# Kernel tuning notes

Hardware: AMD Instinct MI355X
Metric: run time of the kernel (lower is better)

Reference implementation:

```python
import jax, jax.numpy as jnp
import numpy as np

B, SEQ, D, H = 4, 128, 64, 512
EPS = 1e-6


def setup_inputs() -> dict:
    key = jax.random.key(0)
    ks = jax.random.split(key, 7)
    sc = lambda fan_in: 1.0 / np.sqrt(fan_in)
    return {
        "x": jax.random.normal(ks[0], (B, SEQ, D), dtype=jnp.float32),
        "W1": jax.random.normal(ks[1], (D, H), dtype=jnp.float32) * sc(D),
        "b1": jax.random.normal(ks[2], (H,), dtype=jnp.float32) * sc(D),
        "W2": jax.random.normal(ks[3], (H, H), dtype=jnp.float32) * sc(H),
        "b2": jax.random.normal(ks[4], (H,), dtype=jnp.float32) * sc(H),
        "W3": jax.random.normal(ks[5], (H, D * D), dtype=jnp.float32) * sc(H),
        "b3": jax.random.normal(ks[6], (D * D,), dtype=jnp.float32) * sc(H),
    }


def _geometry(x, W1, b1, W2, b2, W3, b3):
    d = W1.shape[0]
    # LearnableMetricTensor: MLP on mean-pooled tokens -> Cholesky-like PD metric
    h = x.mean(axis=1)                                  # [B, d]
    h = jax.nn.relu(h @ W1 + b1)
    h = jax.nn.relu(h @ W2 + b2)
    L = jnp.tril((h @ W3 + b3).reshape(-1, d, d))       # [B, d, d]
    G = L @ jnp.swapaxes(L, -1, -2) + EPS * jnp.eye(d, dtype=x.dtype)
    Ginv = jnp.linalg.inv(G)

    # Christoffel symbols (vectorized form of the per-(i,j,k) loop):
    # Gamma[b,i,j,k] = 0.5 * sum_m Ginv[b,i,m] * (G[b,(m-1)%d,k] + G[b,j,(m-1)%d] - G[b,j,k])
    A = jnp.roll(G, 1, axis=1)                          # A[b,m,k] = G[b,(m-1)%d,k]
    Bm = jnp.roll(G, 1, axis=2)                         # Bm[b,j,m] = G[b,j,(m-1)%d]
    T1 = jnp.einsum('bim,bmk->bik', Ginv, A)            # depends on (i,k)
    T2 = jnp.einsum('bim,bjm->bij', Ginv, Bm)           # depends on (i,j)
    s = Ginv.sum(axis=-1)                               # [B, i]
    Gamma = 0.5 * (T1[:, :, None, :] + T2[:, :, :, None]
                   - s[:, :, None, None] * G[:, None, :, :])  # [B, i, j, k]

    # Riemann tensor (vectorized form of the quadruple loop):
    # partial terms use torch.roll along the batch dim, as in the source
    Dp = jnp.roll(Gamma, 1, axis=0) - Gamma             # Dp[b,i,j,l]
    conn1 = jnp.einsum('bimk,bmjl->bijkl', Gamma, Gamma)
    riemann = (Dp[:, :, :, None, :] - Dp[:, :, :, :, None]
               + conn1 - jnp.swapaxes(conn1, 3, 4))      # [B, i, j, k, l]

    ricci = jnp.einsum('bkikj->bij', riemann)
    scalar_curv = jnp.einsum('bij,bij->b', ricci, Ginv)
    return G, Gamma, riemann, ricci, scalar_curv


def reference(x, W1, b1, W2, b2, W3, b3):
    G, Gamma, riemann, ricci, scalar_curv = _geometry(x, W1, b1, W2, b2, W3, b3)
    return (G, Gamma, riemann, ricci, scalar_curv, x)
```

## Files before the change

kernel.cpp:

```cpp
#include <hip/hip_runtime.h>


#define EPSF 1e-6f

typedef unsigned short u16;
typedef __attribute__((ext_vector_type(8))) short short8v;
typedef __attribute__((ext_vector_type(4))) float f32x4v;
typedef __attribute__((ext_vector_type(2))) double d64x2;

__device__ __forceinline__ u16 f2bf_rne(float f) {
  unsigned u = __float_as_uint(f);
  return (u16)((u + 0x7FFFu + ((u >> 16) & 1u)) >> 16);
}

__global__ void k_mlp_a(const float* __restrict__ x,
                        const float* __restrict__ W1, const float* __restrict__ b1,
                        float* __restrict__ h1out) {
  int b = blockIdx.x;
  int t = threadIdx.x;
  __shared__ float h0[64];
  if (t < 64) {
    const float* xb = x + b * 8192;
    float s = 0.f;
    #pragma unroll 8
    for (int q = 0; q < 128; ++q) s += xb[q * 64 + t];
    h0[t] = s * (1.f / 128.f);
  }
  __syncthreads();
  float acc = b1[t];
  #pragma unroll 8
  for (int d = 0; d < 64; ++d) acc = fmaf(h0[d], W1[d * 512 + t], acc);
  h1out[b * 512 + t] = fmaxf(acc, 0.f);
}

__global__ void k_h2(const float* __restrict__ h1all, const float* __restrict__ W2,
                     const float* __restrict__ b2, float* __restrict__ h2out) {
  int o0 = blockIdx.x * 64, b = blockIdx.y;
  int t = threadIdx.x;
  __shared__ float h1[512];
  __shared__ float red[4][64];
  for (int k = t; k < 512; k += 256) h1[k] = h1all[b * 512 + k];
  __syncthreads();
  int o = o0 + (t & 63), q = t >> 6;
  float acc = 0.f;
  #pragma unroll 8
  for (int k = q * 128; k < q * 128 + 128; ++k)
    acc = fmaf(h1[k], W2[k * 512 + o], acc);
  red[q][t & 63] = acc;
  __syncthreads();
  if (t < 64) {
    float v = red[0][t] + red[1][t] + red[2][t] + red[3][t] + b2[o0 + t];
    h2out[b * 512 + o0 + t] = fmaxf(v, 0.f);
  }
}

__global__ void k_L2(const float* __restrict__ h2all, const float* __restrict__ W3,
                     const float* __restrict__ b3, float* __restrict__ Lout) {
  int t = threadIdx.x;
  int le = t & 127, half = t >> 7;
  int e = blockIdx.x * 128 + le;
  __shared__ float h[4][512];
  __shared__ float red[4][2][128];
  for (int k = t; k < 2048; k += 256) h[k >> 9][k & 511] = h2all[k];
  __syncthreads();
  int i = e >> 6, j = e & 63;
  float a0 = 0.f, a1 = 0.f, a2 = 0.f, a3 = 0.f;
  if (j <= i) {
    const float* w = W3 + (size_t)half * 256 * 4096 + e;
    const float* hh = &h[0][half * 256];
    #pragma unroll 8
    for (int k = 0; k < 256; ++k) {
      float wv = w[(size_t)k * 4096];
      a0 = fmaf(hh[k], wv, a0);
      a1 = fmaf(hh[512 + k], wv, a1);
      a2 = fmaf(hh[1024 + k], wv, a2);
      a3 = fmaf(hh[1536 + k], wv, a3);
    }
  }
  red[0][half][le] = a0; red[1][half][le] = a1;
  red[2][half][le] = a2; red[3][half][le] = a3;
  __syncthreads();
  if (half == 0) {
    float keep = (j <= i) ? 1.f : 0.f;
    float bb = keep * b3[e];
    #pragma unroll
    for (int bi = 0; bi < 4; ++bi)
      Lout[bi * 4096 + e] = keep * (red[bi][0][le] + red[bi][1][le]) + bb;
  }
}

__global__ void k_G(const float* __restrict__ Lin, float* __restrict__ Gout) {
  int b = blockIdx.x;
  __shared__ float Ls[64 * 65];
  for (int e = threadIdx.x; e < 4096; e += 256)
    Ls[(e >> 6) * 65 + (e & 63)] = Lin[b * 4096 + e];
  __syncthreads();
  for (int p = 0; p < 16; ++p) {
    int e = p * 256 + threadIdx.x;
    int i = e >> 6, j = e & 63;
    float acc = (i == j) ? EPSF : 0.f;
    for (int k = 0; k < 64; ++k) acc = fmaf(Ls[i * 65 + k], Ls[j * 65 + k], acc);
    Gout[b * 4096 + e] = acc;
  }
}

__global__ void k_inv(const float* __restrict__ G, float* __restrict__ Ginv) {
  int b = blockIdx.x;
  int t = threadIdx.x;
  __shared__ double M[64][128];
  __shared__ double prbuf[2][128];
  __shared__ double pvbuf[2];
  int cl = (t & 63) * 2;
  int R0 = (t >> 6) * 16;
  for (int e = t; e < 64 * 128; e += 256) {
    int i = e >> 7, jj = e & 127;
    double v;
    if (jj < 64) v = (double)G[b * 4096 + i * 64 + jj];
    else         v = (jj - 64 == i) ? 1.0 : 0.0;
    M[i][jj] = v;
  }
  __syncthreads();
  if (t < 64) {
    prbuf[0][2 * t]     = M[0][2 * t];
    prbuf[0][2 * t + 1] = M[0][2 * t + 1];
  }
  if (t == 0) pvbuf[0] = M[0][0];
  __syncthreads();
  for (int p = 0; p < 64; ++p) {
    int cur = p & 1, nxt = cur ^ 1;
    double pv   = pvbuf[cur];
    double prv0 = prbuf[cur][cl];
    double prv1 = prbuf[cur][cl + 1];
    double fac[16];
    d64x2 av[16];
    #pragma unroll
    for (int q = 0; q < 16; ++q) fac[q] = M[R0 + q][p];
    #pragma unroll
    for (int q = 0; q < 16; ++q) av[q] = *(const d64x2*)&M[R0 + q][cl];
    double pivinv = 1.0 / pv;
    #pragma unroll
    for (int q = 0; q < 16; ++q) {
      int r = R0 + q;
      double f = (r == p) ? (1.0 - pivinv) : fac[q] * pivinv;
      double n0 = av[q].x - f * prv0;
      double n1 = av[q].y - f * prv1;
      d64x2 nv; nv.x = n0; nv.y = n1;
      *(d64x2*)&M[r][cl] = nv;
      if (r == p + 1) {
        prbuf[nxt][cl]     = n0;
        prbuf[nxt][cl + 1] = n1;
        if (cl == ((p + 1) & 62)) pvbuf[nxt] = ((p + 1) & 1) ? n1 : n0;
      }
    }
    __syncthreads();
  }
  for (int e = t; e < 4096; e += 256)
    Ginv[b * 4096 + e] = (float)M[e >> 6][64 + (e & 63)];
}

__global__ void k_gamma2(const float* __restrict__ G, const float* __restrict__ Ginv,
                         float* __restrict__ GammaOut) {
  int i = blockIdx.x, b = blockIdx.y;
  int t = threadIdx.x;
  __shared__ float Gs[64 * 65];
  __shared__ float gi[64];
  __shared__ float T1[64];
  __shared__ float T2[64];
  __shared__ float svs;
  for (int e = t; e < 4096; e += 256)
    Gs[(e >> 6) * 65 + (e & 63)] = G[b * 4096 + e];
  if (t < 64) gi[t] = Ginv[b * 4096 + i * 64 + t];
  __syncthreads();
  if (t < 64) {
    float acc = 0.f, acc2 = 0.f;
    #pragma unroll 8
    for (int m = 0; m < 64; ++m) {
      acc  = fmaf(gi[m], Gs[((m - 1) & 63) * 65 + t], acc);
      acc2 = fmaf(gi[m], Gs[t * 65 + ((m - 1) & 63)], acc2);
    }
    T1[t] = acc;
    T2[t] = acc2;
    if (t == 0) {
      float s = 0.f;
      for (int m = 0; m < 64; ++m) s += gi[m];
      svs = s;
    }
  }
  __syncthreads();
  float sv = svs;
  float* o = GammaOut + b * 262144 + i * 4096;
  #pragma unroll
  for (int p = 0; p < 16; ++p) {
    int e = p * 256 + t;
    int jj = e >> 6, k = e & 63;
    o[e] = 0.5f * (T1[k] + T2[jj] - sv * Gs[jj * 65 + k]);
  }
}

__global__ void k_prep2(const float* __restrict__ Gamma,
                        u16* __restrict__ Tah, u16* __restrict__ Tal,
                        u16* __restrict__ Tbh, u16* __restrict__ Tbl,
                        const float* __restrict__ x, float* __restrict__ Xout) {
  int s = blockIdx.x, b = blockIdx.y;
  int t = threadIdx.x;
  __shared__ float Ls[64 * 65];
  {
    int gblk = b * 64 + s;
    if (t < 128) Xout[gblk * 128 + t] = x[gblk * 128 + t];
  }
  const float* Gb = Gamma + b * 262144;
  int base = (b * 64 + s) << 12;
  for (int p = 0; p < 16; ++p) {
    int e = p * 256 + t;
    Ls[(e >> 6) * 65 + (e & 63)] = Gb[s * 4096 + e];
  }
  __syncthreads();
  for (int p = 0; p < 16; ++p) {
    int e = p * 256 + t;
    int k = e >> 6, m = e & 63;
    float f = Ls[m * 65 + k];
    u16 hi = f2bf_rne(f);
    float fl = f - __uint_as_float(((unsigned)hi) << 16);
    u16 lo = f2bf_rne(fl);
    Tah[base + e] = hi;
    Tal[base + e] = lo;
  }
  __syncthreads();
  for (int p = 0; p < 16; ++p) {
    int e = p * 256 + t;
    int m = e >> 6, l = e & 63;
    Ls[m * 65 + l] = Gb[m * 4096 + s * 64 + l];
  }
  __syncthreads();
  for (int p = 0; p < 16; ++p) {
    int e = p * 256 + t;
    int l = e >> 6, m = e & 63;
    float f = Ls[m * 65 + l];
    u16 hi = f2bf_rne(f);
    float fl = f - __uint_as_float(((unsigned)hi) << 16);
    u16 lo = f2bf_rne(fl);
    int idx = base + l * 64 + (((m >> 3) ^ (l & 7)) << 3) + (m & 7);
    Tbh[idx] = hi;
    Tbl[idx] = lo;
  }
}

__global__ void k_riemann2(const float* __restrict__ Gamma,
                           const u16* __restrict__ Tah, const u16* __restrict__ Tal,
                           const u16* __restrict__ Tbh, const u16* __restrict__ Tbl,
                           float* __restrict__ R) {
  int j = blockIdx.x, i = blockIdx.y, b = blockIdx.z;
  int t = threadIdx.x;
  __shared__ __align__(16) char smem[64 * 68 * 4];
  __shared__ float dvec[64];
  u16* sBh = (u16*)smem;
  u16* sBl = sBh + 4096;
  float* sU = (float*)smem;

  {
    const u16* pbh = Tbh + ((b * 64 + j) << 12);
    const u16* pbl = Tbl + ((b * 64 + j) << 12);
    #pragma unroll
    for (int p = 0; p < 2; ++p) {
      int g = (p << 8) + t;
      *(short8v*)(sBh + (g << 3)) = *(const short8v*)(pbh + (g << 3));
      *(short8v*)(sBl + (g << 3)) = *(const short8v*)(pbl + (g << 3));
    }
  }
  if (t < 64) {
    const float* Gp = Gamma + ((b + 3) & 3) * 262144 + i * 4096 + j * 64;
    const float* Gc = Gamma + b * 262144 + i * 4096 + j * 64;
    dvec[t] = Gp[t] - Gc[t];
  }

  int lane = t & 63, wv = t >> 6;
  int li = lane & 15, lg = lane >> 4;
  const u16* tah = Tah + (((b * 64 + i) << 12) + (16 * wv + li) * 64 + 8 * lg);
  const u16* tal = Tal + (((b * 64 + i) << 12) + (16 * wv + li) * 64 + 8 * lg);
  short8v aH0 = *(const short8v*)(tah);
  short8v aH1 = *(const short8v*)(tah + 32);
  short8v aL0 = *(const short8v*)(tal);
  short8v aL1 = *(const short8v*)(tal + 32);

  __syncthreads();

  f32x4v acc[4];
  #pragma unroll
  for (int tc = 0; tc < 4; ++tc) {
    acc[tc] = (f32x4v){0.f, 0.f, 0.f, 0.f};
    int rb = 16 * tc + li;
    int rx = rb & 7;
    int off0 = rb * 64 + ((lg ^ rx) << 3);
    int off1 = rb * 64 + (((4 + lg) ^ rx) << 3);
    short8v bH0 = *(const short8v*)(sBh + off0);
    short8v bL0 = *(const short8v*)(sBl + off0);
    short8v bH1 = *(const short8v*)(sBh + off1);
    short8v bL1 = *(const short8v*)(sBl + off1);
    acc[tc] = __builtin_amdgcn_mfma_f32_16x16x32_bf16(aH0, bH0, acc[tc], 0, 0, 0);
    acc[tc] = __builtin_amdgcn_mfma_f32_16x16x32_bf16(aL0, bH0, acc[tc], 0, 0, 0);
    acc[tc] = __builtin_amdgcn_mfma_f32_16x16x32_bf16(aH0, bL0, acc[tc], 0, 0, 0);
    acc[tc] = __builtin_amdgcn_mfma_f32_16x16x32_bf16(aH1, bH1, acc[tc], 0, 0, 0);
    acc[tc] = __builtin_amdgcn_mfma_f32_16x16x32_bf16(aL1, bH1, acc[tc], 0, 0, 0);
    acc[tc] = __builtin_amdgcn_mfma_f32_16x16x32_bf16(aH1, bL1, acc[tc], 0, 0, 0);
  }
  __syncthreads();
  #pragma unroll
  for (int tc = 0; tc < 4; ++tc) {
    #pragma unroll
    for (int r = 0; r < 4; ++r)
      sU[(16 * wv + 4 * lg + r) * 68 + 16 * tc + li] = acc[tc][r];
  }
  __syncthreads();

  int tx = t & 15, ty = t >> 4;
  int l0 = 4 * tx, k0 = 4 * ty;
  float mir[4][4];
  #pragma unroll
  for (int r = 0; r < 4; ++r) {
    float4 v = *(const float4*)(sU + (l0 + r) * 68 + k0);
    mir[r][0] = v.x; mir[r][1] = v.y; mir[r][2] = v.z; mir[r][3] = v.w;
  }
  float dl0 = dvec[l0], dl1 = dvec[l0 + 1], dl2 = dvec[l0 + 2], dl3 = dvec[l0 + 3];
  float* Rout = R + (((size_t)((b * 64 + i) * 64 + j)) << 12);
  #pragma unroll
  for (int q = 0; q < 4; ++q) {
    float4 uq = *(const float4*)(sU + (k0 + q) * 68 + l0);
    float dk = dvec[k0 + q];
    float4 o;
    o.x = uq.x - mir[0][q] + dl0 - dk;
    o.y = uq.y - mir[1][q] + dl1 - dk;
    o.z = uq.z - mir[2][q] + dl2 - dk;
    o.w = uq.w - mir[3][q] + dl3 - dk;
    *(float4*)(Rout + (k0 + q) * 64 + l0) = o;
  }
}

__global__ void k_riemann_f32(const float* __restrict__ Gamma, float* __restrict__ R) {
  int j = blockIdx.x, i = blockIdx.y, b = blockIdx.z;
  int t = threadIdx.x;
  __shared__ float Ai[64 * 64];
  __shared__ float Bj[64 * 64];
  __shared__ float U[64 * 65];
  __shared__ float dvec[64];
  const float* Gb = Gamma + b * 262144;
  const float* Gbi = Gb + i * 4096;
  for (int e = t; e < 4096; e += 256) Ai[e] = Gbi[e];
  for (int e = t; e < 4096; e += 256) {
    int m = e >> 6, l = e & 63;
    Bj[e] = Gb[m * 4096 + j * 64 + l];
  }
  if (t < 64) {
    const float* Gp = Gamma + ((b + 3) & 3) * 262144 + i * 4096 + j * 64;
    dvec[t] = Gp[t] - Gbi[j * 64 + t];
  }
  __syncthreads();
  int tx = t & 15, ty = t >> 4;
  int k0 = ty * 4, l0 = tx * 4;
  float acc[4][4] = {{0.f}};
  for (int m = 0; m < 64; ++m) {
    float4 a = *(const float4*)(Ai + m * 64 + k0);
    float4 bb = *(const float4*)(Bj + m * 64 + l0);
    acc[0][0] = fmaf(a.x, bb.x, acc[0][0]); acc[0][1] = fmaf(a.x, bb.y, acc[0][1]);
    acc[0][2] = fmaf(a.x, bb.z, acc[0][2]); acc[0][3] = fmaf(a.x, bb.w, acc[0][3]);
    acc[1][0] = fmaf(a.y, bb.x, acc[1][0]); acc[1][1] = fmaf(a.y, bb.y, acc[1][1]);
    acc[1][2] = fmaf(a.y, bb.z, acc[1][2]); acc[1][3] = fmaf(a.y, bb.w, acc[1][3]);
    acc[2][0] = fmaf(a.z, bb.x, acc[2][0]); acc[2][1] = fmaf(a.z, bb.y, acc[2][1]);
    acc[2][2] = fmaf(a.z, bb.z, acc[2][2]); acc[2][3] = fmaf(a.z, bb.w, acc[2][3]);
    acc[3][0] = fmaf(a.w, bb.x, acc[3][0]); acc[3][1] = fmaf(a.w, bb.y, acc[3][1]);
    acc[3][2] = fmaf(a.w, bb.z, acc[3][2]); acc[3][3] = fmaf(a.w, bb.w, acc[3][3]);
  }
  for (int q = 0; q < 4; ++q)
    for (int r = 0; r < 4; ++r)
      U[(k0 + q) * 65 + (l0 + r)] = acc[q][r];
  __syncthreads();
  float* Rout = R + (((size_t)((b * 64 + i) * 64 + j)) << 12);
  for (int q = 0; q < 4; ++q) {
    int k = k0 + q;
    float dk = dvec[k];
    float4 o;
    o.x = acc[q][0] - U[(l0 + 0) * 65 + k] + dvec[l0 + 0] - dk;
    o.y = acc[q][1] - U[(l0 + 1) * 65 + k] + dvec[l0 + 1] - dk;
    o.z = acc[q][2] - U[(l0 + 2) * 65 + k] + dvec[l0 + 2] - dk;
    o.w = acc[q][3] - U[(l0 + 3) * 65 + k] + dvec[l0 + 3] - dk;
    *(float4*)(Rout + k * 64 + l0) = o;
  }
}

__global__ void k_ricci3(const float* __restrict__ Gamma, float* __restrict__ ricci) {
  int i = blockIdx.x, b = blockIdx.y;
  int t = threadIdx.x;
  int j = t & 63, q = t >> 6;
  __shared__ float sC[64][65];
  __shared__ float redA[4][64];
  __shared__ float redS[4][64];
  __shared__ float redP[4][64];
  __shared__ float sPc[64];
  __shared__ float tmpP[64];
  const float* Gb = Gamma + b * 262144;
  int bp = (b + 3) & 3;
  const float* Gp = Gamma + bp * 262144;
  for (int e = t; e < 4096; e += 256) {
    int m = e >> 6, k = e & 63;
    sC[m][k] = Gb[m * 4096 + i * 64 + k];
  }
  if (t < 64) tmpP[t] = Gp[t * 4096 + i * 64 + t];
  __syncthreads();
  float a4p = 0.f, sgp = 0.f, pcp = 0.f;
  for (int mm = 0; mm < 16; ++mm) {
    int m = q * 16 + mm;
    const float* col = Gb + m * 64 + j;
    float partial = 0.f;
    #pragma unroll 8
    for (int k = 0; k < 64; ++k)
      partial = fmaf(sC[m][k], col[(size_t)k * 4096], partial);
    a4p += partial;
    sgp += Gp[m * 4096 + i * 64 + j];
    pcp += Gb[m * 4097 + j * 64];
  }
  redA[q][j] = a4p;
  redS[q][j] = sgp;
  redP[q][j] = pcp;
  __syncthreads();
  if (t < 64) sPc[t] = redP[0][t] + redP[1][t] + redP[2][t] + redP[3][t];
  __syncthreads();
  if (t < 64) {
    float a4  = redA[0][t] + redA[1][t] + redA[2][t] + redA[3][t];
    float SGp = redS[0][t] + redS[1][t] + redS[2][t] + redS[3][t];
    float SGc = 0.f, a3 = 0.f;
    #pragma unroll 8
    for (int m = 0; m < 64; ++m) {
      SGc += sC[m][t];
      a3 = fmaf(sPc[m], sC[m][t], a3);
    }
    float Ppi = 0.f;
    #pragma unroll 8
    for (int s = 0; s < 64; ++s) Ppi += tmpP[s];
    ricci[b * 4096 + i * 64 + t] = (SGp - SGc) - (Ppi - sPc[i]) + a3 - a4;
  }
}

__global__ void k_scal(const float* __restrict__ ricci, const float* __restrict__ Ginv,
                       float* __restrict__ scal) {
  int b = blockIdx.x;
  int t = threadIdx.x;
  __shared__ float red[256];
  float local = 0.f;
  for (int e = t; e < 4096; e += 256) local += ricci[b * 4096 + e] * Ginv[b * 4096 + e];
  red[t] = local;
  __syncthreads();
  for (int off = 128; off > 0; off >>= 1) {
    if (t < off) red[t] += red[t + off];
    __syncthreads();
  }
  if (t == 0) scal[b] = red[0];
}

__global__ void k_copy(const float* __restrict__ x, float* __restrict__ out) {
  int idx = blockIdx.x * 256 + threadIdx.x;
  out[idx] = x[idx];
}

extern "C" void kernel_launch(void* const* d_in, const int* in_sizes, int n_in,
                              void* d_out, int out_size, void* d_ws, size_t ws_size,
                              hipStream_t stream) {
  const float* x  = (const float*)d_in[0];
  const float* W1 = (const float*)d_in[1];
  const float* b1 = (const float*)d_in[2];
  const float* W2 = (const float*)d_in[3];
  const float* b2 = (const float*)d_in[4];
  const float* W3 = (const float*)d_in[5];
  const float* b3 = (const float*)d_in[6];

  float* out   = (float*)d_out;
  float* G     = out;
  float* Gamma = out + 16384;
  float* Riem  = out + 1064960;
  float* Ricci = out + 68173824;
  float* Scal  = out + 68190208;
  float* Xout  = out + 68190212;

  float* ws   = (float*)d_ws;
  float* h1   = ws;
  float* Lbuf = ws + 2048;
  float* h2   = ws + 18432;
  float* Ginv = ws + 18432;
  u16* Tah = (u16*)(ws + 34816);
  u16* Tal = Tah + (1 << 20);
  u16* Tbh = Tal + (1 << 20);
  u16* Tbl = Tbh + (1 << 20);
  const size_t need = 34816u * 4u + 4u * (1u << 21);

  hipLaunchKernelGGL(k_mlp_a, dim3(4),     dim3(512), 0, stream, x, W1, b1, h1);
  hipLaunchKernelGGL(k_h2,    dim3(8, 4),  dim3(256), 0, stream, h1, W2, b2, h2);
  hipLaunchKernelGGL(k_L2,    dim3(32),    dim3(256), 0, stream, h2, W3, b3, Lbuf);
  hipLaunchKernelGGL(k_G,     dim3(4),     dim3(256), 0, stream, Lbuf, G);
  hipLaunchKernelGGL(k_inv,   dim3(4),     dim3(256), 0, stream, G, Ginv);
  hipLaunchKernelGGL(k_gamma2, dim3(64, 4), dim3(256), 0, stream, G, Ginv, Gamma);
  hipLaunchKernelGGL(k_ricci3, dim3(64, 4), dim3(256), 0, stream, Gamma, Ricci);
  hipLaunchKernelGGL(k_scal,   dim3(4),     dim3(256), 0, stream, Ricci, Ginv, Scal);
  if (ws_size >= need) {
    hipLaunchKernelGGL(k_prep2,    dim3(64, 4),     dim3(256), 0, stream,
                       Gamma, Tah, Tal, Tbh, Tbl, x, Xout);
    hipLaunchKernelGGL(k_riemann2, dim3(64, 64, 4), dim3(256), 0, stream,
                       Gamma, Tah, Tal, Tbh, Tbl, Riem);
  } else {
    hipLaunchKernelGGL(k_copy,        dim3(128),       dim3(256), 0, stream, x, Xout);
    hipLaunchKernelGGL(k_riemann_f32, dim3(64, 64, 4), dim3(256), 0, stream, Gamma, Riem);
  }
}
```

Baseline: 267.1 us.

## Fuse small kernels to cut launches and fold bf16 split prep into producers

Merges the two front MLP layers into one kernel (recomputing layer 1 per block), folds the x copy into the W3 kernel, merges G construction with the fp64 Gauss-Jordan inverse using a shared-memory union, and moves the bf16 hi/lo split of Gamma into the gamma and ricci kernels so the separate prep pass and its re-read of Gamma disappear. The aim is to reduce kernel launch count and redundant global traffic in a latency-dominated chain. In exchange, the layer-1 work is recomputed in every block, and the gamma and ricci kernels do extra stores.

```diff
diff --git a/kernel.cpp b/kernel.cpp
--- a/kernel.cpp
+++ b/kernel.cpp
@@ -13,12 +13,15 @@
   return (u16)((u + 0x7FFFu + ((u >> 16) & 1u)) >> 16);
 }
 
-__global__ void k_mlp_a(const float* __restrict__ x,
-                        const float* __restrict__ W1, const float* __restrict__ b1,
-                        float* __restrict__ h1out) {
-  int b = blockIdx.x;
+__global__ void k_front2(const float* __restrict__ x,
+                         const float* __restrict__ W1, const float* __restrict__ b1,
+                         const float* __restrict__ W2, const float* __restrict__ b2,
+                         float* __restrict__ h2out) {
+  int o0 = blockIdx.x * 64, b = blockIdx.y;
   int t = threadIdx.x;
   __shared__ float h0[64];
+  __shared__ float h1[512];
+  __shared__ float red[4][64];
   if (t < 64) {
     const float* xb = x + b * 8192;
     float s = 0.f;
@@ -27,19 +30,12 @@
     h0[t] = s * (1.f / 128.f);
   }
   __syncthreads();
-  float acc = b1[t];
-  #pragma unroll 8
-  for (int d = 0; d < 64; ++d) acc = fmaf(h0[d], W1[d * 512 + t], acc);
-  h1out[b * 512 + t] = fmaxf(acc, 0.f);
-}
-
-__global__ void k_h2(const float* __restrict__ h1all, const float* __restrict__ W2,
-                     const float* __restrict__ b2, float* __restrict__ h2out) {
-  int o0 = blockIdx.x * 64, b = blockIdx.y;
-  int t = threadIdx.x;
-  __shared__ float h1[512];
-  __shared__ float red[4][64];
-  for (int k = t; k < 512; k += 256) h1[k] = h1all[b * 512 + k];
+  for (int k = t; k < 512; k += 256) {
+    float acc = b1[k];
+    #pragma unroll 8
+    for (int d = 0; d < 64; ++d) acc = fmaf(h0[d], W1[d * 512 + k], acc);
+    h1[k] = fmaxf(acc, 0.f);
+  }
   __syncthreads();
   int o = o0 + (t & 63), q = t >> 6;
   float acc = 0.f;
@@ -54,9 +50,14 @@
   }
 }
 
-__global__ void k_L2(const float* __restrict__ h2all, const float* __restrict__ W3,
-                     const float* __restrict__ b3, float* __restrict__ Lout) {
-  int t = threadIdx.x;
+__global__ void k_L2x(const float* __restrict__ h2all, const float* __restrict__ W3,
+                      const float* __restrict__ b3, float* __restrict__ Lout,
+                      const float* __restrict__ x, float* __restrict__ Xout) {
+  int t = threadIdx.x;
+  {
+    int idx = blockIdx.x * 1024 + t * 4;
+    *(float4*)(Xout + idx) = *(const float4*)(x + idx);
+  }
   int le = t & 127, half = t >> 7;
   int e = blockIdx.x * 128 + le;
   __shared__ float h[4][512];
@@ -89,54 +90,56 @@
   }
 }
 
-__global__ void k_G(const float* __restrict__ Lin, float* __restrict__ Gout) {
+__global__ void k_invG(const float* __restrict__ Lin, float* __restrict__ Gout,
+                       float* __restrict__ Ginv) {
   int b = blockIdx.x;
-  __shared__ float Ls[64 * 65];
-  for (int e = threadIdx.x; e < 4096; e += 256)
-    Ls[(e >> 6) * 65 + (e & 63)] = Lin[b * 4096 + e];
-  __syncthreads();
+  int t = threadIdx.x;
+  __shared__ union {
+    float Ls[64 * 65];
+    struct { double M[64][128]; double prbuf[2][128]; double pvbuf[2]; } inv;
+  } sm;
+  for (int e = t; e < 4096; e += 256)
+    sm.Ls[(e >> 6) * 65 + (e & 63)] = Lin[b * 4096 + e];
+  __syncthreads();
+  float Gv[16];
+  #pragma unroll
   for (int p = 0; p < 16; ++p) {
-    int e = p * 256 + threadIdx.x;
+    int e = p * 256 + t;
     int i = e >> 6, j = e & 63;
     float acc = (i == j) ? EPSF : 0.f;
-    for (int k = 0; k < 64; ++k) acc = fmaf(Ls[i * 65 + k], Ls[j * 65 + k], acc);
+    #pragma unroll 8
+    for (int k = 0; k < 64; ++k) acc = fmaf(sm.Ls[i * 65 + k], sm.Ls[j * 65 + k], acc);
+    Gv[p] = acc;
     Gout[b * 4096 + e] = acc;
   }
-}
-
-__global__ void k_inv(const float* __restrict__ G, float* __restrict__ Ginv) {
-  int b = blockIdx.x;
-  int t = threadIdx.x;
-  __shared__ double M[64][128];
-  __shared__ double prbuf[2][128];
-  __shared__ double pvbuf[2];
+  __syncthreads();
+  #pragma unroll
+  for (int p = 0; p < 16; ++p) {
+    int e = p * 256 + t;
+    int i = e >> 6, j = e & 63;
+    sm.inv.M[i][j] = (double)Gv[p];
+    sm.inv.M[i][64 + j] = (i == j) ? 1.0 : 0.0;
+  }
+  __syncthreads();
+  if (t < 64) {
+    sm.inv.prbuf[0][2 * t]     = sm.inv.M[0][2 * t];
+    sm.inv.prbuf[0][2 * t + 1] = sm.inv.M[0][2 * t + 1];
+  }
+  if (t == 0) sm.inv.pvbuf[0] = sm.inv.M[0][0];
+  __syncthreads();
   int cl = (t & 63) * 2;
   int R0 = (t >> 6) * 16;
-  for (int e = t; e < 64 * 128; e += 256) {
-    int i = e >> 7, jj = e & 127;
-    double v;
-    if (jj < 64) v = (double)G[b * 4096 + i * 64 + jj];
-    else         v = (jj - 64 == i) ? 1.0 : 0.0;
-    M[i][jj] = v;
-  }
-  __syncthreads();
-  if (t < 64) {
-    prbuf[0][2 * t]     = M[0][2 * t];
-    prbuf[0][2 * t + 1] = M[0][2 * t + 1];
-  }
-  if (t == 0) pvbuf[0] = M[0][0];
-  __syncthreads();
   for (int p = 0; p < 64; ++p) {
     int cur = p & 1, nxt = cur ^ 1;
-    double pv   = pvbuf[cur];
-    double prv0 = prbuf[cur][cl];
-    double prv1 = prbuf[cur][cl + 1];
+    double pv   = sm.inv.pvbuf[cur];
+    double prv0 = sm.inv.prbuf[cur][cl];
+    double prv1 = sm.inv.prbuf[cur][cl + 1];
     double fac[16];
     d64x2 av[16];
     #pragma unroll
-    for (int q = 0; q < 16; ++q) fac[q] = M[R0 + q][p];
-    #pragma unroll
-    for (int q = 0; q < 16; ++q) av[q] = *(const d64x2*)&M[R0 + q][cl];
+    for (int q = 0; q < 16; ++q) fac[q] = sm.inv.M[R0 + q][p];
+    #pragma unroll
+    for (int q = 0; q < 16; ++q) av[q] = *(const d64x2*)&sm.inv.M[R0 + q][cl];
     double pivinv = 1.0 / pv;
     #pragma unroll
     for (int q = 0; q < 16; ++q) {
@@ -145,24 +148,26 @@
       double n0 = av[q].x - f * prv0;
       double n1 = av[q].y - f * prv1;
       d64x2 nv; nv.x = n0; nv.y = n1;
-      *(d64x2*)&M[r][cl] = nv;
+      *(d64x2*)&sm.inv.M[r][cl] = nv;
       if (r == p + 1) {
-        prbuf[nxt][cl]     = n0;
-        prbuf[nxt][cl + 1] = n1;
-        if (cl == ((p + 1) & 62)) pvbuf[nxt] = ((p + 1) & 1) ? n1 : n0;
+        sm.inv.prbuf[nxt][cl]     = n0;
+        sm.inv.prbuf[nxt][cl + 1] = n1;
+        if (cl == ((p + 1) & 62)) sm.inv.pvbuf[nxt] = ((p + 1) & 1) ? n1 : n0;
       }
     }
     __syncthreads();
   }
   for (int e = t; e < 4096; e += 256)
-    Ginv[b * 4096 + e] = (float)M[e >> 6][64 + (e & 63)];
-}
-
-__global__ void k_gamma2(const float* __restrict__ G, const float* __restrict__ Ginv,
-                         float* __restrict__ GammaOut) {
+    Ginv[b * 4096 + e] = (float)sm.inv.M[e >> 6][64 + (e & 63)];
+}
+
+__global__ void k_gamma3(const float* __restrict__ G, const float* __restrict__ Ginv,
+                         float* __restrict__ GammaOut,
+                         u16* __restrict__ Tah, u16* __restrict__ Tal) {
   int i = blockIdx.x, b = blockIdx.y;
   int t = threadIdx.x;
   __shared__ float Gs[64 * 65];
+  __shared__ float Tt[64 * 65];
   __shared__ float gi[64];
   __shared__ float T1[64];
   __shared__ float T2[64];
@@ -193,56 +198,110 @@
   for (int p = 0; p < 16; ++p) {
     int e = p * 256 + t;
     int jj = e >> 6, k = e & 63;
-    o[e] = 0.5f * (T1[k] + T2[jj] - sv * Gs[jj * 65 + k]);
-  }
-}
-
-__global__ void k_prep2(const float* __restrict__ Gamma,
-                        u16* __restrict__ Tah, u16* __restrict__ Tal,
-                        u16* __restrict__ Tbh, u16* __restrict__ Tbl,
-                        const float* __restrict__ x, float* __restrict__ Xout) {
-  int s = blockIdx.x, b = blockIdx.y;
-  int t = threadIdx.x;
-  __shared__ float Ls[64 * 65];
-  {
-    int gblk = b * 64 + s;
-    if (t < 128) Xout[gblk * 128 + t] = x[gblk * 128 + t];
-  }
+    float val = 0.5f * (T1[k] + T2[jj] - sv * Gs[jj * 65 + k]);
+    o[e] = val;
+    Tt[jj * 65 + k] = val;
+  }
+  __syncthreads();
+  if (Tah) {
+    int base = (b * 64 + i) << 12;
+    #pragma unroll
+    for (int p = 0; p < 16; ++p) {
+      int e = p * 256 + t;
+      int k = e >> 6, m = e & 63;
+      float f = Tt[m * 65 + k];
+      u16 hi = f2bf_rne(f);
+      float fl = f - __uint_as_float(((unsigned)hi) << 16);
+      u16 lo = f2bf_rne(fl);
+      Tah[base + e] = hi;
+      Tal[base + e] = lo;
+    }
+  }
+}
+
+__global__ void k_ricci4(const float* __restrict__ Gamma, float* __restrict__ ricci,
+                         u16* __restrict__ Tbh, u16* __restrict__ Tbl) {
+  int i = blockIdx.x, b = blockIdx.y;
+  int t = threadIdx.x;
+  int j = t & 63, q = t >> 6;
+  __shared__ float sC[64][65];
+  __shared__ float redA[4][64];
+  __shared__ float redS[4][64];
+  __shared__ float redP[4][64];
+  __shared__ float sPc[64];
+  __shared__ float tmpP[64];
   const float* Gb = Gamma + b * 262144;
-  int base = (b * 64 + s) << 12;
-  for (int p = 0; p < 16; ++p) {
-    int e = p * 256 + t;
-    Ls[(e >> 6) * 65 + (e & 63)] = Gb[s * 4096 + e];
-  }
-  __syncthreads();
-  for (int p = 0; p < 16; ++p) {
-    int e = p * 256 + t;
-    int k = e >> 6, m = e & 63;
-    float f = Ls[m * 65 + k];
-    u16 hi = f2bf_rne(f);
-    float fl = f - __uint_as_float(((unsigned)hi) << 16);
-    u16 lo = f2bf_rne(fl);
-    Tah[base + e] = hi;
-    Tal[base + e] = lo;
-  }
-  __syncthreads();
-  for (int p = 0; p < 16; ++p) {
-    int e = p * 256 + t;
-    int m = e >> 6, l = e & 63;
-    Ls[m * 65 + l] = Gb[m * 4096 + s * 64 + l];
-  }
-  __syncthreads();
-  for (int p = 0; p < 16; ++p) {
-    int e = p * 256 + t;
-    int l = e >> 6, m = e & 63;
-    float f = Ls[m * 65 + l];
-    u16 hi = f2bf_rne(f);
-    float fl = f - __uint_as_float(((unsigned)hi) << 16);
-    u16 lo = f2bf_rne(fl);
-    int idx = base + l * 64 + (((m >> 3) ^ (l & 7)) << 3) + (m & 7);
-    Tbh[idx] = hi;
-    Tbl[idx] = lo;
-  }
+  int bp = (b + 3) & 3;
+  const float* Gp = Gamma + bp * 262144;
+  for (int e = t; e < 4096; e += 256) {
+    int m = e >> 6, k = e & 63;
+    sC[m][k] = Gb[m * 4096 + i * 64 + k];
+  }
+  if (t < 64) tmpP[t] = Gp[t * 4096 + i * 64 + t];
+  __syncthreads();
+  float a4p = 0.f, sgp = 0.f, pcp = 0.f;
+  for (int mm = 0; mm < 16; ++mm) {
+    int m = q * 16 + mm;
+    const float* col = Gb + m * 64 + j;
+    float partial = 0.f;
+    #pragma unroll 8
+    for (int k = 0; k < 64; ++k)
+      partial = fmaf(sC[m][k], col[(size_t)k * 4096], partial);
+    a4p += partial;
+    sgp += Gp[m * 4096 + i * 64 + j];
+    pcp += Gb[m * 4097 + j * 64];
+  }
+  redA[q][j] = a4p;
+  redS[q][j] = sgp;
+  redP[q][j] = pcp;
+  __syncthreads();
+  if (t < 64) sPc[t] = redP[0][t] + redP[1][t] + redP[2][t] + redP[3][t];
+  __syncthreads();
+  if (t < 64) {
+    float a4  = redA[0][t] + redA[1][t] + redA[2][t] + redA[3][t];
+    float SGp = redS[0][t] + redS[1][t] + redS[2][t] + redS[3][t];
+    float SGc = 0.f, a3 = 0.f;
+    #pragma unroll 8
+    for (int m = 0; m < 64; ++m) {
+      SGc += sC[m][t];
+      a3 = fmaf(sPc[m], sC[m][t], a3);
+    }
+    float Ppi = 0.f;
+    #pragma unroll 8
+    for (int s = 0; s < 64; ++s) Ppi += tmpP[s];
+    ricci[b * 4096 + i * 64 + t] = (SGp - SGc) - (Ppi - sPc[i]) + a3 - a4;
+  }
+  if (Tbh) {
+    int base = (b * 64 + i) << 12;
+    #pragma unroll
+    for (int p = 0; p < 16; ++p) {
+      int e = p * 256 + t;
+      int l = e >> 6, m = e & 63;
+      float f = sC[m][l];
+      u16 hi = f2bf_rne(f);
+      float fl = f - __uint_as_float(((unsigned)hi) << 16);
+      u16 lo = f2bf_rne(fl);
+      int idx = base + l * 64 + (((m >> 3) ^ (l & 7)) << 3) + (m & 7);
+      Tbh[idx] = hi;
+      Tbl[idx] = lo;
+    }
+  }
+}
+
+__global__ void k_scal(const float* __restrict__ ricci, const float* __restrict__ Ginv,
+                       float* __restrict__ scal) {
+  int b = blockIdx.x;
+  int t = threadIdx.x;
+  __shared__ float red[256];
+  float local = 0.f;
+  for (int e = t; e < 4096; e += 256) local += ricci[b * 4096 + e] * Ginv[b * 4096 + e];
+  red[t] = local;
+  __syncthreads();
+  for (int off = 128; off > 0; off >>= 1) {
+    if (t < off) red[t] += red[t + off];
+    __syncthreads();
+  }
+  if (t == 0) scal[b] = red[0];
 }
 
 __global__ void k_riemann2(const float* __restrict__ Gamma,
@@ -386,80 +445,6 @@
   }
 }
 
-__global__ void k_ricci3(const float* __restrict__ Gamma, float* __restrict__ ricci) {
-  int i = blockIdx.x, b = blockIdx.y;
-  int t = threadIdx.x;
-  int j = t & 63, q = t >> 6;
-  __shared__ float sC[64][65];
-  __shared__ float redA[4][64];
-  __shared__ float redS[4][64];
-  __shared__ float redP[4][64];
-  __shared__ float sPc[64];
-  __shared__ float tmpP[64];
-  const float* Gb = Gamma + b * 262144;
-  int bp = (b + 3) & 3;
-  const float* Gp = Gamma + bp * 262144;
-  for (int e = t; e < 4096; e += 256) {
-    int m = e >> 6, k = e & 63;
-    sC[m][k] = Gb[m * 4096 + i * 64 + k];
-  }
-  if (t < 64) tmpP[t] = Gp[t * 4096 + i * 64 + t];
-  __syncthreads();
-  float a4p = 0.f, sgp = 0.f, pcp = 0.f;
-  for (int mm = 0; mm < 16; ++mm) {
-    int m = q * 16 + mm;
-    const float* col = Gb + m * 64 + j;
-    float partial = 0.f;
-    #pragma unroll 8
-    for (int k = 0; k < 64; ++k)
-      partial = fmaf(sC[m][k], col[(size_t)k * 4096], partial);
-    a4p += partial;
-    sgp += Gp[m * 4096 + i * 64 + j];
-    pcp += Gb[m * 4097 + j * 64];
-  }
-  redA[q][j] = a4p;
-  redS[q][j] = sgp;
-  redP[q][j] = pcp;
-  __syncthreads();
-  if (t < 64) sPc[t] = redP[0][t] + redP[1][t] + redP[2][t] + redP[3][t];
-  __syncthreads();
-  if (t < 64) {
-    float a4  = redA[0][t] + redA[1][t] + redA[2][t] + redA[3][t];
-    float SGp = redS[0][t] + redS[1][t] + redS[2][t] + redS[3][t];
-    float SGc = 0.f, a3 = 0.f;
-    #pragma unroll 8
-    for (int m = 0; m < 64; ++m) {
-      SGc += sC[m][t];
-      a3 = fmaf(sPc[m], sC[m][t], a3);
-    }
-    float Ppi = 0.f;
-    #pragma unroll 8
-    for (int s = 0; s < 64; ++s) Ppi += tmpP[s];
-    ricci[b * 4096 + i * 64 + t] = (SGp - SGc) - (Ppi - sPc[i]) + a3 - a4;
-  }
-}
-
-__global__ void k_scal(const float* __restrict__ ricci, const float* __restrict__ Ginv,
-                       float* __restrict__ scal) {
-  int b = blockIdx.x;
-  int t = threadIdx.x;
-  __shared__ float red[256];
-  float local = 0.f;
-  for (int e = t; e < 4096; e += 256) local += ricci[b * 4096 + e] * Ginv[b * 4096 + e];
-  red[t] = local;
-  __syncthreads();
-  for (int off = 128; off > 0; off >>= 1) {
-    if (t < off) red[t] += red[t + off];
-    __syncthreads();
-  }
-  if (t == 0) scal[b] = red[0];
-}
-
-__global__ void k_copy(const float* __restrict__ x, float* __restrict__ out) {
-  int idx = blockIdx.x * 256 + threadIdx.x;
-  out[idx] = x[idx];
-}
-
 extern "C" void kernel_launch(void* const* d_in, const int* in_sizes, int n_in,
                               void* d_out, int out_size, void* d_ws, size_t ws_size,
                               hipStream_t stream) {
@@ -480,31 +465,28 @@
   float* Xout  = out + 68190212;
 
   float* ws   = (float*)d_ws;
-  float* h1   = ws;
+  float* h2   = ws;
   float* Lbuf = ws + 2048;
-  float* h2   = ws + 18432;
   float* Ginv = ws + 18432;
   u16* Tah = (u16*)(ws + 34816);
   u16* Tal = Tah + (1 << 20);
   u16* Tbh = Tal + (1 << 20);
   u16* Tbl = Tbh + (1 << 20);
   const size_t need = 34816u * 4u + 4u * (1u << 21);
-
-  hipLaunchKernelGGL(k_mlp_a, dim3(4),     dim3(512), 0, stream, x, W1, b1, h1);
-  hipLaunchKernelGGL(k_h2,    dim3(8, 4),  dim3(256), 0, stream, h1, W2, b2, h2);
-  hipLaunchKernelGGL(k_L2,    dim3(32),    dim3(256), 0, stream, h2, W3, b3, Lbuf);
-  hipLaunchKernelGGL(k_G,     dim3(4),     dim3(256), 0, stream, Lbuf, G);
-  hipLaunchKernelGGL(k_inv,   dim3(4),     dim3(256), 0, stream, G, Ginv);
-  hipLaunchKernelGGL(k_gamma2, dim3(64, 4), dim3(256), 0, stream, G, Ginv, Gamma);
-  hipLaunchKernelGGL(k_ricci3, dim3(64, 4), dim3(256), 0, stream, Gamma, Ricci);
+  bool mfma = (ws_size >= need);
+
+  hipLaunchKernelGGL(k_front2, dim3(8, 4),  dim3(256), 0, stream, x, W1, b1, W2, b2, h2);
+  hipLaunchKernelGGL(k_L2x,    dim3(32),    dim3(256), 0, stream, h2, W3, b3, Lbuf, x, Xout);
+  hipLaunchKernelGGL(k_invG,   dim3(4),     dim3(256), 0, stream, Lbuf, G, Ginv);
+  hipLaunchKernelGGL(k_gamma3, dim3(64, 4), dim3(256), 0, stream, G, Ginv, Gamma,
+                     mfma ? Tah : (u16*)nullptr, mfma ? Tal : (u16*)nullptr);
+  hipLaunchKernelGGL(k_ricci4, dim3(64, 4), dim3(256), 0, stream, Gamma, Ricci,
+                     mfma ? Tbh : (u16*)nullptr, mfma ? Tbl : (u16*)nullptr);
   hipLaunchKernelGGL(k_scal,   dim3(4),     dim3(256), 0, stream, Ricci, Ginv, Scal);
-  if (ws_size >= need) {
-    hipLaunchKernelGGL(k_prep2,    dim3(64, 4),     dim3(256), 0, stream,
-                       Gamma, Tah, Tal, Tbh, Tbl, x, Xout);
+  if (mfma) {
     hipLaunchKernelGGL(k_riemann2, dim3(64, 64, 4), dim3(256), 0, stream,
                        Gamma, Tah, Tal, Tbh, Tbl, Riem);
   } else {
-    hipLaunchKernelGGL(k_copy,        dim3(128),       dim3(256), 0, stream, x, Xout);
     hipLaunchKernelGGL(k_riemann_f32, dim3(64, 64, 4), dim3(256), 0, stream, Gamma, Riem);
   }
 }
```

New measurement: 275.0 us. 1.03x slower.
